# Kernel tuning notes

Hardware: AMD Instinct MI355X
Metric: run time of the kernel (lower is better)

## Reference

```python
import jax, jax.numpy as jnp
import numpy as np

B, T, D_MODEL, N_HEADS = 2, 2048, 1024, 16
HEAD_DIM = D_MODEL // N_HEADS
EPS = 1e-6
ROPE_BASE = 10000.0


def _rope_cos_sin(seq_len, dim, offset=0, dtype=jnp.float32):
    half = dim // 2
    inv_freq = 1.0 / (ROPE_BASE ** (jnp.arange(half, dtype=jnp.float32) / half))
    pos = jnp.arange(offset, offset + seq_len, dtype=jnp.float32)
    freqs = pos[:, None] * inv_freq[None, :]              # (T, half)
    emb = jnp.concatenate([freqs, freqs], axis=-1)        # (T, dim)
    return jnp.cos(emb).astype(dtype), jnp.sin(emb).astype(dtype)


def _rotate_half(x):
    x1, x2 = jnp.split(x, 2, axis=-1)
    return jnp.concatenate([-x2, x1], axis=-1)


def setup_inputs() -> dict:
    key = jax.random.key(0)
    k1, k2, k3 = jax.random.split(key, 3)
    x = jax.random.normal(k1, (B, T, D_MODEL), dtype=jnp.float32)
    norm_w = jnp.ones((D_MODEL,), dtype=jnp.float32)
    w_qkv = jax.random.normal(k2, (3 * D_MODEL, D_MODEL), dtype=jnp.float32) * 0.02
    w_out = jax.random.normal(k3, (D_MODEL, D_MODEL), dtype=jnp.float32) * 0.02
    return {"x": x, "norm_w": norm_w, "w_qkv": w_qkv, "w_out": w_out}


def reference(x, norm_w, w_qkv, w_out):
    # RMSNorm (pre-norm)
    h = x * jax.lax.rsqrt(jnp.mean(jnp.square(x), axis=-1, keepdims=True) + EPS) * norm_w
    # Fused QKV projection: (B,T,3*D)
    qkv = jnp.einsum('btd,ed->bte', h, w_qkv).reshape(B, T, 3, N_HEADS, HEAD_DIM)
    q, k, v = qkv[:, :, 0], qkv[:, :, 1], qkv[:, :, 2]   # each (B,T,H,Dh)
    # RoPE on q, k (offset=0)
    cos, sin = _rope_cos_sin(T, HEAD_DIM, dtype=q.dtype)
    cos = cos[None, :, None, :]
    sin = sin[None, :, None, :]
    q = q * cos + _rotate_half(q) * sin
    k = k * cos + _rotate_half(k) * sin
    # Causal scaled dot-product attention
    scale = 1.0 / np.sqrt(HEAD_DIM)
    scores = jnp.einsum('bqhd,bkhd->bhqk', q, k) * scale  # (B,H,T,T)
    causal = jnp.tril(jnp.ones((T, T), dtype=bool))
    scores = jnp.where(causal[None, None], scores, jnp.finfo(scores.dtype).min)
    attn = jax.nn.softmax(scores, axis=-1)
    out = jnp.einsum('bhqk,bkhd->bqhd', attn, v).reshape(B, T, D_MODEL)
    out = jnp.einsum('btd,ed->bte', out, w_out)
    return x + out
```

## Files before the change

### kernel.cpp

```cpp
#include <hip/hip_runtime.h>
#include <math.h>

typedef unsigned short u16;
typedef unsigned int u32;
typedef __attribute__((ext_vector_type(4))) float f32x4;
typedef __attribute__((ext_vector_type(8))) short s16x8;

#define GLL16(g, l) __builtin_amdgcn_global_load_lds( \
    (const __attribute__((address_space(1))) void*)(g), \
    (__attribute__((address_space(3))) void*)(l), 16, 0, 0)

#define MFMA16(a, b, c) __builtin_amdgcn_mfma_f32_16x16x32_bf16(a, b, c, 0, 0, 0)

__device__ __forceinline__ u16 f2bf(float f) {
  union { float f; u32 u; } v; v.f = f;
  u32 r = v.u + 0x7FFFu + ((v.u >> 16) & 1u);
  return (u16)(r >> 16);
}
__device__ __forceinline__ float bf2f(u16 h) {
  union { u32 u; float f; } v; v.u = ((u32)h) << 16;
  return v.f;
}
__device__ __forceinline__ u32 pk2bf(float lo, float hi) {
  union { float f; u32 u; } a, b; a.f = lo; b.f = hi;
  return __builtin_amdgcn_perm(b.u + 0x8000u, a.u + 0x8000u, 0x07060302u);
}
__device__ __forceinline__ float fexp2(float x) {
#if __has_builtin(__builtin_amdgcn_exp2f)
  return __builtin_amdgcn_exp2f(x);
#else
  return exp2f(x);
#endif
}

__global__ __launch_bounds__(256) void prep_kernel(const float* __restrict__ x,
                                                   const float* __restrict__ wgt,
                                                   const float* __restrict__ w_qkv,
                                                   const float* __restrict__ w_out,
                                                   u16* __restrict__ h,
                                                   u16* __restrict__ wqkv_b,
                                                   u16* __restrict__ wout_b) {
  __shared__ float red[4];
  const int bid = blockIdx.x, tid = threadIdx.x;
  if (bid < 4096) {
    const int row = bid;
    const float4 v = *(const float4*)&x[(size_t)row * 1024 + tid * 4];
    float ss = v.x * v.x + v.y * v.y + v.z * v.z + v.w * v.w;
    ss += __shfl_xor(ss, 1);  ss += __shfl_xor(ss, 2);  ss += __shfl_xor(ss, 4);
    ss += __shfl_xor(ss, 8);  ss += __shfl_xor(ss, 16); ss += __shfl_xor(ss, 32);
    if ((tid & 63) == 0) red[tid >> 6] = ss;
    __syncthreads();
    const float tot = red[0] + red[1] + red[2] + red[3];
    const float s = rsqrtf(tot * (1.0f / 1024.0f) + 1e-6f);
    const float4 g = *(const float4*)&wgt[tid * 4];
    uint2 o;
    o.x = (u32)f2bf(v.x * s * g.x) | ((u32)f2bf(v.y * s * g.y) << 16);
    o.y = (u32)f2bf(v.z * s * g.z) | ((u32)f2bf(v.w * s * g.w) << 16);
    *(uint2*)&h[(size_t)row * 1024 + tid * 4] = o;
  } else if (bid < 7168) {
    int i = (bid - 4096) * 256 + tid;
    float4 v = ((const float4*)w_qkv)[i];
    uint2 o;
    o.x = (u32)f2bf(v.x) | ((u32)f2bf(v.y) << 16);
    o.y = (u32)f2bf(v.z) | ((u32)f2bf(v.w) << 16);
    ((uint2*)wqkv_b)[i] = o;
  } else {
    int i = (bid - 7168) * 256 + tid;
    float4 v = ((const float4*)w_out)[i];
    uint2 o;
    o.x = (u32)f2bf(v.x) | ((u32)f2bf(v.y) << 16);
    o.y = (u32)f2bf(v.z) | ((u32)f2bf(v.w) << 16);
    ((uint2*)wout_b)[i] = o;
  }
}

template <int EPI>
__global__ __launch_bounds__(256) void gemm_bt(const u16* __restrict__ A,
                                               const u16* __restrict__ Bt,
                                               u16* __restrict__ Cb,
                                               float* __restrict__ Cf,
                                               const float* __restrict__ resid,
                                               int M, int N, int K) {
  __shared__ __attribute__((aligned(16))) u16 As[128 * 32];
  __shared__ __attribute__((aligned(16))) u16 Bs[128 * 32];
  const int tid = threadIdx.x;
  const int w = tid >> 6, lane = tid & 63;
  const int quad = lane >> 4, l16 = lane & 15;
  const int gm0 = blockIdx.y * 128, gn0 = blockIdx.x * 128;
  const int wm = (w & 1) * 64, wn = (w >> 1) * 64;

  f32x4 acc[4][4] = {};

  for (int k0 = 0; k0 < K; k0 += 32) {
    __syncthreads();
    if (w < 2) {
      #pragma unroll
      for (int i = 0; i < 4; ++i) {
        int sb = (w * 4 + i) * 64;
        int slot = sb + lane;
        int m = slot >> 2, c = (slot & 3) ^ (m & 3);
        GLL16(A + (size_t)(gm0 + m) * K + k0 + c * 8, &As[sb * 8]);
      }
    } else {
      #pragma unroll
      for (int i = 0; i < 4; ++i) {
        int sb = ((w - 2) * 4 + i) * 64;
        int slot = sb + lane;
        int n = slot >> 2, c = (slot & 3) ^ (n & 3);
        GLL16(Bt + (size_t)(gn0 + n) * K + k0 + c * 8, &Bs[sb * 8]);
      }
    }
    __syncthreads();
    s16x8 aF[4], bF[4];
    #pragma unroll
    for (int i = 0; i < 4; ++i) {
      int m = wm + i * 16 + l16;
      aF[i] = *(const s16x8*)&As[(m * 4 + (quad ^ (m & 3))) * 8];
    }
    #pragma unroll
    for (int j = 0; j < 4; ++j) {
      int n = wn + j * 16 + l16;
      bF[j] = *(const s16x8*)&Bs[(n * 4 + (quad ^ (n & 3))) * 8];
    }
    #pragma unroll
    for (int i = 0; i < 4; ++i)
      #pragma unroll
      for (int j = 0; j < 4; ++j)
        acc[i][j] = MFMA16(aF[i], bF[j], acc[i][j]);
  }

  #pragma unroll
  for (int i = 0; i < 4; ++i) {
    int row0 = gm0 + wm + i * 16 + quad * 4;
    #pragma unroll
    for (int j = 0; j < 4; ++j) {
      int col = gn0 + wn + j * 16 + l16;
      #pragma unroll
      for (int r = 0; r < 4; ++r) {
        size_t idx = (size_t)(row0 + r) * N + col;
        if (EPI == 0) Cb[idx] = f2bf(acc[i][j][r]);
        else          Cf[idx] = acc[i][j][r] + resid[idx];
      }
    }
  }
}

__global__ __launch_bounds__(512, 2) void gemm256(const u16* __restrict__ A,
                                                  const u16* __restrict__ Bt,
                                                  u16* __restrict__ Cb) {
  __shared__ __attribute__((aligned(16))) char smem[131072];
  const int tid = threadIdx.x;
  const int w = tid >> 6, lane = tid & 63;
  const int quad = lane >> 4, l16 = lane & 15;
  const int wr = w >> 2, wc = w & 3;
  const int rsw = l16 & 7;
  const int id = blockIdx.x;
  const int sw = (id & 7) * 24 + (id >> 3);
  const int by = sw / 12, bx = sw - by * 12;
  const int gm0 = by * 256, gn0 = bx * 256;
  const int scg = (lane & 7) ^ (lane >> 3);

  auto STAGE_HALF = [&](int kt, int part) {
    const int sb = (kt & 1) * 65536 + (part >> 1) * 32768 + (part & 1) * 16384;
    const u16* src = (part >> 1) ? Bt : A;
    const int g0 = ((part >> 1) ? gn0 : gm0) + (part & 1) * 128;
    const int k0 = kt * 64;
    #pragma unroll
    for (int q = 0; q < 2; ++q) {
      int r = q * 64 + (tid >> 3);
      GLL16(src + (size_t)(g0 + r) * 1024 + k0 + scg * 8,
            smem + sb + q * 8192 + w * 1024);
    }
  };

  f32x4 acc[8][4] = {};

  STAGE_HALF(0, 0); STAGE_HALF(0, 1);
  STAGE_HALF(0, 2); STAGE_HALF(0, 3);
  STAGE_HALF(1, 2); STAGE_HALF(1, 3);
  asm volatile("s_waitcnt vmcnt(4)" ::: "memory");
  __builtin_amdgcn_s_barrier();

  for (int kt = 0; kt < 16; ++kt) {
    const char* Ab = smem + (kt & 1) * 65536;
    const char* Bb = Ab + 32768;
    const int arow = wr * 128 + l16;
    const int brow = wc * 64 + l16;
    s16x8 aA[4][2], bB[4][2];

    #pragma unroll
    for (int fi = 0; fi < 4; ++fi) {
      const char* p = Ab + (arow + fi * 16) * 128;
      aA[fi][0] = *(const s16x8*)(p + ((quad ^ rsw) * 16));
      aA[fi][1] = *(const s16x8*)(p + (((4 + quad) ^ rsw) * 16));
    }
    #pragma unroll
    for (int fj = 0; fj < 4; ++fj) {
      const char* p = Bb + (brow + fj * 16) * 128;
      bB[fj][0] = *(const s16x8*)(p + ((quad ^ rsw) * 16));
      bB[fj][1] = *(const s16x8*)(p + (((4 + quad) ^ rsw) * 16));
    }

    if (kt < 15) { STAGE_HALF(kt + 1, 0); STAGE_HALF(kt + 1, 1); }

    __builtin_amdgcn_s_setprio(1);
    #pragma unroll
    for (int fi = 0; fi < 4; ++fi)
      #pragma unroll
      for (int fj = 0; fj < 4; ++fj) {
        acc[fi][fj] = MFMA16(aA[fi][0], bB[fj][0], acc[fi][fj]);
        acc[fi][fj] = MFMA16(aA[fi][1], bB[fj][1], acc[fi][fj]);
      }
    __builtin_amdgcn_s_setprio(0);

    #pragma unroll
    for (int fi = 0; fi < 4; ++fi) {
      const char* p = Ab + (arow + (4 + fi) * 16) * 128;
      aA[fi][0] = *(const s16x8*)(p + ((quad ^ rsw) * 16));
      aA[fi][1] = *(const s16x8*)(p + (((4 + quad) ^ rsw) * 16));
    }

    __builtin_amdgcn_s_setprio(1);
    #pragma unroll
    for (int fi = 0; fi < 4; ++fi)
      #pragma unroll
      for (int fj = 0; fj < 4; ++fj) {
        acc[4 + fi][fj] = MFMA16(aA[fi][0], bB[fj][0], acc[4 + fi][fj]);
        acc[4 + fi][fj] = MFMA16(aA[fi][1], bB[fj][1], acc[4 + fi][fj]);
      }
    __builtin_amdgcn_s_setprio(0);

    __builtin_amdgcn_s_barrier();

    if (kt < 14) {
      STAGE_HALF(kt + 2, 2); STAGE_HALF(kt + 2, 3);
      asm volatile("s_waitcnt vmcnt(4)" ::: "memory");
    } else if (kt == 14) {
      asm volatile("s_waitcnt vmcnt(0)" ::: "memory");
    }
    __builtin_amdgcn_s_barrier();
  }

  #pragma unroll
  for (int g = 0; g < 8; ++g) {
    const int row0 = gm0 + wr * 128 + g * 16 + quad * 4;
    #pragma unroll
    for (int fj = 0; fj < 4; ++fj) {
      const int col = gn0 + wc * 64 + fj * 16 + l16;
      #pragma unroll
      for (int r = 0; r < 4; ++r)
        Cb[(size_t)(row0 + r) * 3072 + col] = f2bf(acc[g][fj][r]);
    }
  }
}

__global__ __launch_bounds__(256) void rope_kernel(const u16* __restrict__ qkv,
                                                   u16* __restrict__ Qr,
                                                   u16* __restrict__ Kr,
                                                   u16* __restrict__ Vt) {
  const int tt = blockIdx.x, bh = blockIdx.y;
  const int b = bh >> 4, h = bh & 15;
  const int tid = threadIdx.x;
  const float QSCALE = 0.125f * 1.4426950408889634f;

  #pragma unroll
  for (int ii = 0; ii < 8; ++ii) {
    int idx = ii * 256 + tid;
    int tl = idx >> 5, jj = idx & 31;
    int t = tt * 64 + tl;
    size_t mrow = (size_t)(b * 2048 + t) * 3072 + h * 64;
    float q1 = bf2f(qkv[mrow + jj]),        q2 = bf2f(qkv[mrow + 32 + jj]);
    float k1 = bf2f(qkv[mrow + 1024 + jj]), k2 = bf2f(qkv[mrow + 1024 + 32 + jj]);
    float invf = exp2f(-(float)jj * (13.287712379549449f / 32.0f));
    float ang = (float)t * invf;
    float sn, cs;
    sincosf(ang, &sn, &cs);
    size_t orow = (size_t)(bh * 2048 + t) * 64;
    Qr[orow + jj]      = f2bf((q1 * cs - q2 * sn) * QSCALE);
    Qr[orow + 32 + jj] = f2bf((q2 * cs + q1 * sn) * QSCALE);
    Kr[orow + jj]      = f2bf(k1 * cs - k2 * sn);
    Kr[orow + 32 + jj] = f2bf(k2 * cs + k1 * sn);
  }

  __shared__ __attribute__((aligned(16))) u16 Vl[64][72];
  for (int s = tid; s < 512; s += 256) {
    int r = s >> 3, c8 = (s & 7) * 8;
    *(uint4*)&Vl[r][c8] =
        *(const uint4*)&qkv[(size_t)(b * 2048 + tt * 64 + r) * 3072 + 2048 + h * 64 + c8];
  }
  __syncthreads();
  for (int s = tid; s < 512; s += 256) {
    int d = s >> 3, t8 = (s & 7) * 8;
    u16 tmp[8];
    #pragma unroll
    for (int k = 0; k < 8; ++k) tmp[k] = Vl[t8 + k][d];
    *(uint4*)&Vt[(size_t)(bh * 64 + d) * 2048 + tt * 64 + t8] = *(uint4*)tmp;
  }
}

__global__ __launch_bounds__(512, 2) void attn_kernel(const u16* __restrict__ Qr,
                                                      const u16* __restrict__ Kr,
                                                      const u16* __restrict__ Vt,
                                                      u16* __restrict__ AO) {
  __shared__ __attribute__((aligned(16))) char smem[102400];
  const int tid = threadIdx.x;
  const int w = tid >> 6, lane = tid & 63;
  const int wq = w & 3, wp = w >> 2;
  const int quad = lane >> 4, l16 = lane & 15;
  const int id = blockIdx.x;
  const int bh = id & 31;
  const int c  = id >> 5;
  const int b = bh >> 4, h = bh & 15;
  const size_t qkb = (size_t)bh * (2048 * 64);
  const size_t vtb = (size_t)bh * (64 * 2048);
  u16* Pw = (u16*)(smem + 65536 + w * 4608);

  const int srow = lane >> 3;
  const int scg  = (lane & 7) ^ srow;
  const int smat = w & 1, stp = (w >> 1) & 1, shalf = (w >> 2) & 1;

  auto STAGE = [&](int j0, int d) {
    const int jn = j0 + stp;
    if (smat == 0) {
      #pragma unroll
      for (int ii = 0; ii < 4; ++ii) {
        int i = shalf * 4 + ii;
        GLL16(Kr + qkb + (size_t)(jn * 64 + i * 8 + srow) * 64 + scg * 8,
              smem + (stp * 2 + d) * 8192 + i * 1024);
      }
    } else {
      #pragma unroll
      for (int ii = 0; ii < 4; ++ii) {
        int i = shalf * 4 + ii;
        GLL16(Vt + vtb + (size_t)(i * 8 + srow) * 2048 + jn * 64 + scg * 8,
              smem + 32768 + (stp * 2 + d) * 8192 + i * 1024);
      }
    }
  };

  for (int t = 0; t < 2; ++t) {
    const int qblk = t ? (15 - c) : c;
    const int q0w = qblk * 128 + wq * 32;
    const int steps = qblk + 1;

    s16x8 bQ[2][2];
    #pragma unroll
    for (int s = 0; s < 2; ++s)
      #pragma unroll
      for (int hf = 0; hf < 2; ++hf)
        bQ[s][hf] = *(const s16x8*)&Qr[qkb + (size_t)(q0w + s * 16 + l16) * 64 + hf * 32 + quad * 8];

    f32x4 O[2][4] = {};
    float l_run[2] = {0.0f, 0.0f};

    STAGE(0, 0);
    __syncthreads();

    for (int st = 0; st < steps; ++st) {
      const int cur = st & 1;
      if (st + 1 < steps) STAGE(2 * st + 2, cur ^ 1);

      const int j = 2 * st + wp;
      if (j * 64 <= q0w + 31) {
        const u16* Kb = (const u16*)(smem + (wp * 2 + cur) * 8192);
        const u16* Vb = (const u16*)(smem + 32768 + (wp * 2 + cur) * 8192);
        const bool masked = (j * 64 + 63 > q0w);
        const int rsw = (l16 & 7);

        s16x8 aK[4][2];
        #pragma unroll
        for (int kt = 0; kt < 4; ++kt)
          #pragma unroll
          for (int hf = 0; hf < 2; ++hf)
            aK[kt][hf] = *(const s16x8*)&Kb[(kt * 16 + l16) * 64 + (((hf * 4 + quad) ^ rsw) * 8)];

        f32x4 S[2][4];
        __builtin_amdgcn_s_setprio(1);
        #pragma unroll
        for (int kt = 0; kt < 4; ++kt)
          #pragma unroll
          for (int s = 0; s < 2; ++s) {
            f32x4 z = {};
            z = MFMA16(aK[kt][0], bQ[s][0], z);
            S[s][kt] = MFMA16(aK[kt][1], bQ[s][1], z);
          }
        __builtin_amdgcn_s_setprio(0);

        if (masked) {
          #pragma unroll
          for (int s = 0; s < 2; ++s) {
            int q = q0w + s * 16 + l16;
            #pragma unroll
            for (int kt = 0; kt < 4; ++kt) {
              int key0 = j * 64 + kt * 16 + quad * 4;
              #pragma unroll
              for (int r = 0; r < 4; ++r)
                if (key0 + r > q) S[s][kt][r] = -1e30f;
            }
          }
        }

        #pragma unroll
        for (int s = 0; s < 2; ++s) {
          float sum = 0.0f;
          #pragma unroll
          for (int kt = 0; kt < 4; ++kt) {
            #pragma unroll
            for (int r = 0; r < 4; ++r) {
              float e = fexp2(S[s][kt][r]);
              S[s][kt][r] = e;
              sum += e;
            }
          }
          sum += __shfl_xor(sum, 16);
          sum += __shfl_xor(sum, 32);
          l_run[s] += sum;
          #pragma unroll
          for (int kt = 0; kt < 4; ++kt) {
            uint2 pw;
            pw.x = pk2bf(S[s][kt][0], S[s][kt][1]);
            pw.y = pk2bf(S[s][kt][2], S[s][kt][3]);
            *(uint2*)&Pw[s * 1152 + l16 * 72 + kt * 16 + quad * 4] = pw;
          }
        }

        s16x8 bP[2][2];
        #pragma unroll
        for (int s = 0; s < 2; ++s) {
          bP[s][0] = *(const s16x8*)&Pw[s * 1152 + l16 * 72 + quad * 8];
          bP[s][1] = *(const s16x8*)&Pw[s * 1152 + l16 * 72 + 32 + quad * 8];
        }
        s16x8 aV[4][2];
        #pragma unroll
        for (int dt = 0; dt < 4; ++dt)
          #pragma unroll
          for (int hf = 0; hf < 2; ++hf)
            aV[dt][hf] = *(const s16x8*)&Vb[(dt * 16 + l16) * 64 + (((hf * 4 + quad) ^ rsw) * 8)];

        __builtin_amdgcn_s_setprio(1);
        #pragma unroll
        for (int dt = 0; dt < 4; ++dt)
          #pragma unroll
          for (int s = 0; s < 2; ++s) {
            O[s][dt] = MFMA16(aV[dt][0], bP[s][0], O[s][dt]);
            O[s][dt] = MFMA16(aV[dt][1], bP[s][1], O[s][dt]);
          }
        __builtin_amdgcn_s_setprio(0);
      }

      __syncthreads();
    }

    if (wp == 1) {
      float* Lsl = (float*)(smem + 65536 + wq * 512);
      Lsl[lane]      = l_run[0];
      Lsl[64 + lane] = l_run[1];
      f32x4* slot = (f32x4*)smem + wq * 512;
      #pragma unroll
      for (int s = 0; s < 2; ++s)
        #pragma unroll
        for (int dt = 0; dt < 4; ++dt)
          slot[(s * 4 + dt) * 64 + lane] = O[s][dt];
    }
    __syncthreads();
    if (wp == 0) {
      const float* Lsl = (const float*)(smem + 65536 + wq * 512);
      const f32x4* slot = (const f32x4*)smem + wq * 512;
      #pragma unroll
      for (int s = 0; s < 2; ++s) {
        float l_tot = l_run[s] + Lsl[s * 64 + lane];
        float inv = __builtin_amdgcn_rcpf(l_tot);
        int q = q0w + s * 16 + l16;
        #pragma unroll
        for (int dt = 0; dt < 4; ++dt) {
          f32x4 o = O[s][dt] + slot[(s * 4 + dt) * 64 + lane];
          uint2 ow;
          ow.x = pk2bf(o[0] * inv, o[1] * inv);
          ow.y = pk2bf(o[2] * inv, o[3] * inv);
          *(uint2*)&AO[(size_t)(b * 2048 + q) * 1024 + h * 64 + dt * 16 + quad * 4] = ow;
        }
      }
    }
    __syncthreads();
  }
}

extern "C" void kernel_launch(void* const* d_in, const int* in_sizes, int n_in,
                              void* d_out, int out_size, void* d_ws, size_t ws_size,
                              hipStream_t stream) {
  const float* x      = (const float*)d_in[0];
  const float* norm_w = (const float*)d_in[1];
  const float* w_qkv  = (const float*)d_in[2];
  const float* w_out  = (const float*)d_in[3];
  float* out = (float*)d_out;

  u16* ws     = (u16*)d_ws;
  u16* wqkv_b = ws;
  u16* wout_b = wqkv_b + 3145728;
  u16* h_b    = wout_b + 1048576;
  u16* qkv_b  = h_b + 4194304;
  u16* Qr     = qkv_b + 12582912;
  u16* Kr     = Qr + 4194304;
  u16* Vt     = Kr + 4194304;
  u16* AO     = Vt + 4194304;

  prep_kernel<<<8192, 256, 0, stream>>>(x, norm_w, w_qkv, w_out, h_b, wqkv_b, wout_b);
  gemm256<<<192, 512, 0, stream>>>(h_b, wqkv_b, qkv_b);
  rope_kernel<<<dim3(32, 32), 256, 0, stream>>>(qkv_b, Qr, Kr, Vt);
  attn_kernel<<<256, 512, 0, stream>>>(Qr, Kr, Vt, AO);
  gemm_bt<1><<<dim3(8, 32), 256, 0, stream>>>(AO, wout_b, nullptr, out, x,
                                              4096, 1024, 1024);
}
```

Measured before the change: 183.9 us.

## Fuse RoPE and V transpose into QKV GEMM epilogue

Removes the separate rope kernel and the intermediate qkv buffer. The QKV GEMM epilogue now applies rotary embedding and the softmax scale directly to Q and K accumulators, writing them in head-major layout. V tiles are staged through swizzled shared memory and written transposed. This saves a launch and a full round trip of the qkv tensor through memory, at the cost of sincos work and scattered 2-byte stores in the GEMM epilogue.

```diff
diff --git a/kernel.cpp b/kernel.cpp
--- a/kernel.cpp
+++ b/kernel.cpp
@@ -147,7 +147,9 @@
 
 __global__ __launch_bounds__(512, 2) void gemm256(const u16* __restrict__ A,
                                                   const u16* __restrict__ Bt,
-                                                  u16* __restrict__ Cb) {
+                                                  u16* __restrict__ Qr,
+                                                  u16* __restrict__ Kr,
+                                                  u16* __restrict__ Vt) {
   __shared__ __attribute__((aligned(16))) char smem[131072];
   const int tid = threadIdx.x;
   const int w = tid >> 6, lane = tid & 63;
@@ -241,60 +243,60 @@
     __builtin_amdgcn_s_barrier();
   }
 
-  #pragma unroll
-  for (int g = 0; g < 8; ++g) {
-    const int row0 = gm0 + wr * 128 + g * 16 + quad * 4;
-    #pragma unroll
-    for (int fj = 0; fj < 4; ++fj) {
-      const int col = gn0 + wc * 64 + fj * 16 + l16;
-      #pragma unroll
-      for (int r = 0; r < 4; ++r)
-        Cb[(size_t)(row0 + r) * 3072 + col] = f2bf(acc[g][fj][r]);
-    }
-  }
-}
-
-__global__ __launch_bounds__(256) void rope_kernel(const u16* __restrict__ qkv,
-                                                   u16* __restrict__ Qr,
-                                                   u16* __restrict__ Kr,
-                                                   u16* __restrict__ Vt) {
-  const int tt = blockIdx.x, bh = blockIdx.y;
-  const int b = bh >> 4, h = bh & 15;
-  const int tid = threadIdx.x;
-  const float QSCALE = 0.125f * 1.4426950408889634f;
-
-  #pragma unroll
-  for (int ii = 0; ii < 8; ++ii) {
-    int idx = ii * 256 + tid;
-    int tl = idx >> 5, jj = idx & 31;
-    int t = tt * 64 + tl;
-    size_t mrow = (size_t)(b * 2048 + t) * 3072 + h * 64;
-    float q1 = bf2f(qkv[mrow + jj]),        q2 = bf2f(qkv[mrow + 32 + jj]);
-    float k1 = bf2f(qkv[mrow + 1024 + jj]), k2 = bf2f(qkv[mrow + 1024 + 32 + jj]);
-    float invf = exp2f(-(float)jj * (13.287712379549449f / 32.0f));
-    float ang = (float)t * invf;
-    float sn, cs;
-    sincosf(ang, &sn, &cs);
-    size_t orow = (size_t)(bh * 2048 + t) * 64;
-    Qr[orow + jj]      = f2bf((q1 * cs - q2 * sn) * QSCALE);
-    Qr[orow + 32 + jj] = f2bf((q2 * cs + q1 * sn) * QSCALE);
-    Kr[orow + jj]      = f2bf(k1 * cs - k2 * sn);
-    Kr[orow + 32 + jj] = f2bf(k2 * cs + k1 * sn);
-  }
-
-  __shared__ __attribute__((aligned(16))) u16 Vl[64][72];
-  for (int s = tid; s < 512; s += 256) {
-    int r = s >> 3, c8 = (s & 7) * 8;
-    *(uint4*)&Vl[r][c8] =
-        *(const uint4*)&qkv[(size_t)(b * 2048 + tt * 64 + r) * 3072 + 2048 + h * 64 + c8];
-  }
-  __syncthreads();
-  for (int s = tid; s < 512; s += 256) {
-    int d = s >> 3, t8 = (s & 7) * 8;
-    u16 tmp[8];
-    #pragma unroll
-    for (int k = 0; k < 8; ++k) tmp[k] = Vl[t8 + k][d];
-    *(uint4*)&Vt[(size_t)(bh * 64 + d) * 2048 + tt * 64 + t8] = *(uint4*)tmp;
+  const int bb = gm0 >> 11;
+  const int tt0 = (gm0 & 2047) + wr * 128;
+  if (bx < 8) {
+    const bool isQ = (bx < 4);
+    const int h = ((bx & 3) << 2) + wc;
+    const size_t obase = (size_t)(bb * 16 + h) * (2048 * 64);
+    u16* dst = isQ ? Qr : Kr;
+    const float SC = isQ ? 0.125f * 1.4426950408889634f : 1.0f;
+    #pragma unroll
+    for (int fj = 0; fj < 2; ++fj) {
+      const int jj = fj * 16 + l16;
+      const float invf = exp2f(-(float)jj * (13.287712379549449f / 32.0f));
+      #pragma unroll
+      for (int g = 0; g < 8; ++g) {
+        #pragma unroll
+        for (int r = 0; r < 4; ++r) {
+          const int t = tt0 + g * 16 + quad * 4 + r;
+          float sn, cs;
+          sincosf((float)t * invf, &sn, &cs);
+          const float q1 = acc[g][fj][r], q2 = acc[g][2 + fj][r];
+          dst[obase + (size_t)t * 64 + jj]      = f2bf((q1 * cs - q2 * sn) * SC);
+          dst[obase + (size_t)t * 64 + jj + 32] = f2bf((q2 * cs + q1 * sn) * SC);
+        }
+      }
+    }
+  } else {
+    const int h = ((bx - 8) << 2) + wc;
+    const size_t obase = (size_t)(bb * 16 + h) * 64;
+    u16* Vl = (u16*)smem + wc * 16384;
+    #pragma unroll
+    for (int g = 0; g < 8; ++g)
+      #pragma unroll
+      for (int fj = 0; fj < 4; ++fj) {
+        const int d = fj * 16 + l16;
+        #pragma unroll
+        for (int r = 0; r < 4; ++r) {
+          const int tl = wr * 128 + g * 16 + quad * 4 + r;
+          Vl[tl * 64 + (d ^ (((tl >> 3) & 7) << 3))] = f2bf(acc[g][fj][r]);
+        }
+      }
+    __syncthreads();
+    const int c = lane & 7, lg = lane >> 3;
+    const int tb = gm0 & 2047;
+    #pragma unroll
+    for (int c32 = wr * 2; c32 < wr * 2 + 2; ++c32)
+      #pragma unroll
+      for (int dp = 0; dp < 8; ++dp) {
+        const int d = dp * 8 + lg;
+        const u16* col = Vl + (c32 * 64 + c * 8) * 64 + (d ^ (c << 3));
+        u16 tmp[8];
+        #pragma unroll
+        for (int k = 0; k < 8; ++k) tmp[k] = col[k * 64];
+        *(uint4*)&Vt[(obase + d) * 2048 + tb + c32 * 64 + c * 8] = *(uint4*)tmp;
+      }
   }
 }
 
@@ -498,15 +500,13 @@
   u16* wqkv_b = ws;
   u16* wout_b = wqkv_b + 3145728;
   u16* h_b    = wout_b + 1048576;
-  u16* qkv_b  = h_b + 4194304;
-  u16* Qr     = qkv_b + 12582912;
+  u16* Qr     = h_b + 4194304 + 12582912;
   u16* Kr     = Qr + 4194304;
   u16* Vt     = Kr + 4194304;
   u16* AO     = Vt + 4194304;
 
   prep_kernel<<<8192, 256, 0, stream>>>(x, norm_w, w_qkv, w_out, h_b, wqkv_b, wout_b);
-  gemm256<<<192, 512, 0, stream>>>(h_b, wqkv_b, qkv_b);
-  rope_kernel<<<dim3(32, 32), 256, 0, stream>>>(qkv_b, Qr, Kr, Vt);
+  gemm256<<<192, 512, 0, stream>>>(h_b, wqkv_b, Qr, Kr, Vt);
   attn_kernel<<<256, 512, 0, stream>>>(Qr, Kr, Vt, AO);
   gemm_bt<1><<<dim3(8, 32), 256, 0, stream>>>(AO, wout_b, nullptr, out, x,
                                               4096, 1024, 1024);
```

Result: slower. 221.8 us (+20.6%).
